# Kernel tuning notes

Hardware: AMD Instinct MI355X
Metric: run time of the kernel (lower is better)

The kernel has to match this reference:

```python
import jax, jax.numpy as jnp
import numpy as np

EPS_NORM = 1e-12  # F.normalize eps
EPS_LOG = 1e-10
COMMITMENT_COST = 0.25


def setup_inputs() -> dict:
    key = jax.random.key(0)
    k1, k2 = jax.random.split(key)
    x = jax.random.normal(k1, (32, 256, 32, 32), dtype=jnp.float32)
    # nn.Embedding weight init: uniform(-1, 1)
    W = jax.random.uniform(k2, (1024, 256), dtype=jnp.float32, minval=-1.0, maxval=1.0)
    return {"x": x, "W": W, "n": 2}


def reference(x, W, n):
    sg = jax.lax.stop_gradient
    # NCHW -> NHWC
    inputs = jnp.transpose(x, (0, 2, 3, 1))
    B, H, Wd, D = inputs.shape
    K = W.shape[0]
    flat = inputs.reshape(-1, D)                       # [N, D]
    N = flat.shape[0]
    # squared euclidean distances via matmul: [N, K]
    distances = (jnp.sum(flat * flat, axis=1, keepdims=True)
                 + jnp.sum(W * W, axis=1)
                 - 2.0 * jnp.matmul(flat, W.T))
    # topk of -distances -> n smallest distances
    neg_vals, encoding_indices = jax.lax.top_k(-distances, n)  # [N, n]
    inv_dist = 1.0 / (-neg_vals)                        # 1/distance, [N, n]
    norm = jnp.maximum(jnp.sqrt(jnp.sum(inv_dist * inv_dist, axis=-1, keepdims=True)), EPS_NORM)
    weights = sg(inv_dist / norm)                       # detached in torch
    # scatter weights into one-hot-ish encodings [N, K]
    rows = jnp.arange(N)[:, None]
    encodings = jnp.zeros((N, K), dtype=flat.dtype).at[rows, encoding_indices].set(weights)
    quantized = jnp.matmul(encodings, W).reshape(B, H, Wd, D)
    e_latent_loss = jnp.mean((sg(quantized) - inputs) ** 2)
    q_latent_loss = jnp.mean((quantized - sg(inputs)) ** 2)
    loss = q_latent_loss + COMMITMENT_COST * e_latent_loss
    # straight-through
    quantized_st = inputs + sg(quantized - inputs)
    avg_probs = jnp.mean(encodings, axis=0)
    perplexity = jnp.exp(-jnp.sum(avg_probs * jnp.log(avg_probs + EPS_LOG)))
    return loss, jnp.transpose(quantized_st, (0, 3, 1, 2)), perplexity, encodings
```

## Files before the change

### kernel.cpp

```cpp
#include <hip/hip_runtime.h>
#include <math.h>

#define NROWS 32768
#define DIMS  256
#define KCODES 1024

typedef __attribute__((ext_vector_type(8))) short short8;
typedef __attribute__((ext_vector_type(4))) float f32x4;

#define SWZW(hw) ((((hw) >> 2) & 7) << 2)

static const size_t OFF_WB     = 8388608;
static const size_t OFF_WNORM  = OFF_WB + 131072;
static const size_t OFF_ENCSUM = OFF_WNORM + 1024;
static const size_t OFF_LOSSP  = OFF_ENCSUM + 1024;
static const size_t OFF_WND    = OFF_LOSSP + 8192;

static const size_t OUT_Q    = 1;
static const size_t OUT_PERP = 8388609;
static const size_t OUT_ENC  = 8388610;

__device__ inline unsigned short f2bf(float f) {
    unsigned int u = __float_as_uint(f);
    unsigned int r = u + 0x7FFFu + ((u >> 16) & 1u);
    return (unsigned short)(r >> 16);
}

__device__ inline float packdi(float d, int code) {
    return __uint_as_float((__float_as_uint(d) & 0xFFFFFC00u) | (unsigned)code);
}

__device__ __forceinline__ void gl_lds16(const void* gsrc, void* ldst) {
    typedef const __attribute__((address_space(1))) unsigned int GU;
    typedef __attribute__((address_space(3))) unsigned int LU;
    __builtin_amdgcn_global_load_lds((GU*)gsrc, (LU*)ldst, 16, 0, 0);
}

__global__ __launch_bounds__(256) void wprep(const float* __restrict__ Wm,
                                             unsigned short* __restrict__ Wb,
                                             float* __restrict__ wnorm,
                                             double* __restrict__ wnormd,
                                             float* __restrict__ enc_sum)
{
    const int r = blockIdx.x * 4 + (threadIdx.x >> 6);
    const int lane = threadIdx.x & 63;
    float4 v = ((const float4*)(Wm + (size_t)r * 256))[lane];
    ushort4 o;
    o.x = f2bf(v.x); o.y = f2bf(v.y); o.z = f2bf(v.z); o.w = f2bf(v.w);
    const int d0 = lane * 4;
    const int kk = d0 >> 5, quad = (d0 >> 3) & 3, jb = d0 & 7;
    const int tt = r >> 4, col = r & 15;
    const size_t idx = (size_t)tt * 4096 + (size_t)((kk * 4 + quad) * 16 + col) * 8 + jb;
    *(ushort4*)(Wb + idx) = o;
    double s = (double)v.x*(double)v.x + (double)v.y*(double)v.y
             + (double)v.z*(double)v.z + (double)v.w*(double)v.w;
    #pragma unroll
    for (int off = 32; off > 0; off >>= 1) s += __shfl_down(s, off);
    if (lane == 0) { wnormd[r] = s; wnorm[r] = (float)s; }
    if (blockIdx.x == 0) {
        #pragma unroll
        for (int q = 0; q < 4; ++q) enc_sum[threadIdx.x * 4 + q] = 0.0f;
    }
}

__global__ __launch_bounds__(256, 4) void gemm_topk_quant(
    const float* __restrict__ x, const unsigned short* __restrict__ Wb,
    const float* __restrict__ wnorm, const double* __restrict__ wnd,
    const float* __restrict__ Wm,
    float* __restrict__ enc_sum,
    float* __restrict__ enc,
    float* __restrict__ outq, float* __restrict__ loss_part)
{
    __shared__ __align__(16) char lds[36864];
    float*  sCd   = (float*)lds;
    int*    mIdx  = (int*)(lds + 13312);
    double* rd    = (double*)(lds + 14336);
    float*  qtile = (float*)lds;
    double* rnr   = (double*)(lds + 33792);
    int*    s0    = (int*)(lds + 34048);
    int*    s1    = (int*)(lds + 34176);
    float*  sw0   = (float*)(lds + 34304);
    float*  sw1   = (float*)(lds + 34432);
    double* sredd = (double*)(lds + 34560);
    float*  xbounce = (float*)(lds + 16384);
    float*  wnLds = (float*)(lds + 32768);

    const int t    = threadIdx.x;
    const int wave = t >> 6;
    const int g    = wave & 1;
    const int h    = wave >> 1;
    const int lane = t & 63;
    const int col  = lane & 15;
    const int quad = lane >> 4;
    const int r0   = blockIdx.x * 32;
    const int b    = r0 >> 10;
    const int hw0  = r0 & 1023;
    const float* xblk = x + (size_t)b * 262144 + hw0;

    const int row = t >> 3;
    const int q8  = t & 7;

    const char* wb_bytes = (const char*)Wb;
    {
        const char* src = wb_bytes + (size_t)(h * 32) * 8192 + g * 4096;
        char* dstl = lds + h * 8192 + g * 4096;
        #pragma unroll
        for (int q = 0; q < 4; ++q)
            gl_lds16(src + q * 1024 + lane * 16, dstl + q * 1024);
        gl_lds16((const char*)wnorm + wave * 1024 + lane * 16,
                 (char*)wnLds + wave * 1024);
    }

    float xs[32];
    short8 af[8];
    const int hwq   = t & 7;
    const int dbase = t >> 3;
    const int arow  = g * 16 + col;
    #pragma unroll
    for (int h2 = 0; h2 < 2; ++h2) {
        float4 xv0, xv1, xv2, xv3;
        {
            const float* xp = xblk + hwq * 4;
            xv0 = *(const float4*)(xp + (size_t)(h2 * 128 +  0 + dbase) * 1024);
            xv1 = *(const float4*)(xp + (size_t)(h2 * 128 + 32 + dbase) * 1024);
            xv2 = *(const float4*)(xp + (size_t)(h2 * 128 + 64 + dbase) * 1024);
            xv3 = *(const float4*)(xp + (size_t)(h2 * 128 + 96 + dbase) * 1024);
        }
        if (h2) __syncthreads();
        #pragma unroll
        for (int rr = 0; rr < 4; ++rr) {
            const float4 xv = (rr == 0) ? xv0 : (rr == 1) ? xv1 : (rr == 2) ? xv2 : xv3;
            const int dloc = rr * 32 + dbase;
            #pragma unroll
            for (int j = 0; j < 4; ++j) {
                const int hw = hwq * 4 + j;
                const float vj = (j == 0) ? xv.x : (j == 1) ? xv.y : (j == 2) ? xv.z : xv.w;
                xbounce[(hw * 128 + dloc) ^ SWZW(hw)] = vj;
            }
        }
        __syncthreads();
        #pragma unroll
        for (int c2 = 0; c2 < 4; ++c2) {
            const int w = (row * 128 + c2 * 32 + q8 * 4) ^ SWZW(row);
            f32x4 v = *(const f32x4*)(xbounce + w);
            xs[(h2 * 4 + c2) * 4 + 0] = v.x;
            xs[(h2 * 4 + c2) * 4 + 1] = v.y;
            xs[(h2 * 4 + c2) * 4 + 2] = v.z;
            xs[(h2 * 4 + c2) * 4 + 3] = v.w;
        }
        #pragma unroll
        for (int kk2 = 0; kk2 < 4; ++kk2) {
            const int dloc = kk2 * 32 + quad * 8;
            const int wA = (arow * 128 + dloc) ^ SWZW(arow);
            const int wB = (arow * 128 + dloc + 4) ^ SWZW(arow);
            f32x4 u = *(const f32x4*)(xbounce + wA);
            f32x4 v = *(const f32x4*)(xbounce + wB);
            short8 f;
            f[0] = (short)f2bf(u.x); f[1] = (short)f2bf(u.y);
            f[2] = (short)f2bf(u.z); f[3] = (short)f2bf(u.w);
            f[4] = (short)f2bf(v.x); f[5] = (short)f2bf(v.y);
            f[6] = (short)f2bf(v.z); f[7] = (short)f2bf(v.w);
            af[h2 * 4 + kk2] = f;
        }
    }
    __syncthreads();

    float m0[4], m1[4], m2[4];
    #pragma unroll
    for (int r = 0; r < 4; ++r) { m0[r] = 3.4e38f; m1[r] = 3.4e38f; m2[r] = 3.4e38f; }

    const f32x4 zero4 = {0.f, 0.f, 0.f, 0.f};
    for (int cc = 0; cc < 32; ++cc) {
        if (cc < 31) {
            const char* src = wb_bytes + (size_t)(h * 32 + cc + 1) * 8192 + g * 4096;
            char* dstl = lds + ((cc + 1) & 1) * 16384 + h * 8192 + g * 4096;
            #pragma unroll
            for (int q = 0; q < 4; ++q)
                gl_lds16(src + q * 1024 + lane * 16, dstl + q * 1024);
        }
        *(f32x4*)(enc + (size_t)(r0 + cc) * KCODES + t * 4) = zero4;

        const char* bb = lds + (cc & 1) * 16384 + h * 8192;
        f32x4 acc_a = {0.f, 0.f, 0.f, 0.f};
        f32x4 acc_b = {0.f, 0.f, 0.f, 0.f};
        #pragma unroll
        for (int kk = 0; kk < 4; ++kk) {
            short8 b0 = *(const short8*)(bb + kk * 1024 + lane * 16);
            short8 b1 = *(const short8*)(bb + (kk + 4) * 1024 + lane * 16);
            acc_a = __builtin_amdgcn_mfma_f32_16x16x32_bf16(af[kk], b0, acc_a, 0, 0, 0);
            acc_b = __builtin_amdgcn_mfma_f32_16x16x32_bf16(af[kk + 4], b1, acc_b, 0, 0, 0);
        }
        const int code0 = h * 512 + cc * 16 + col;
        const float wn0 = wnLds[code0];
        #pragma unroll
        for (int r = 0; r < 4; ++r) {
            float pv0 = packdi(fmaf(-2.0f, acc_a[r] + acc_b[r], wn0), code0);
            m2[r] = __builtin_amdgcn_fmed3f(m1[r], m2[r], pv0);
            m1[r] = __builtin_amdgcn_fmed3f(m0[r], m1[r], pv0);
            m0[r] = fminf(m0[r], pv0);
        }
        __syncthreads();
    }

    #pragma unroll
    for (int r = 0; r < 4; ++r) {
        const int rl = g * 16 + quad * 4 + r;
        const int s  = h * 48 + col * 3;
        sCd[(s + 0) * 34 + rl] = m0[r];
        sCd[(s + 1) * 34 + rl] = m1[r];
        sCd[(s + 2) * 34 + rl] = m2[r];
    }
    __syncthreads();

    {
        float a0 = 3.4e38f, a1 = 3.4e38f, a2 = 3.4e38f, a3 = 3.4e38f,
              a4 = 3.4e38f, a5 = 3.4e38f, a6 = 3.4e38f, a7 = 3.4e38f;
        #pragma unroll
        for (int i = 0; i < 12; ++i) {
            float d = sCd[(q8 * 12 + i) * 34 + row];
            if (d < a7) {
                a7 = d; float tf;
                if (a7 < a6) { tf = a7; a7 = a6; a6 = tf; }
                if (a6 < a5) { tf = a6; a6 = a5; a5 = tf; }
                if (a5 < a4) { tf = a5; a5 = a4; a4 = tf; }
                if (a4 < a3) { tf = a4; a4 = a3; a3 = tf; }
                if (a3 < a2) { tf = a3; a3 = a2; a2 = tf; }
                if (a2 < a1) { tf = a2; a2 = a1; a1 = tf; }
                if (a1 < a0) { tf = a1; a1 = a0; a0 = tf; }
            }
        }
        float sel = 3.4e38f;
        #pragma unroll
        for (int q = 0; q < 8; ++q) {
            float m = a0;
            m = fminf(m, __shfl_xor(m, 1));
            m = fminf(m, __shfl_xor(m, 2));
            m = fminf(m, __shfl_xor(m, 4));
            if (q8 == q) sel = m;
            if (a0 == m) { a0 = a1; a1 = a2; a2 = a3; a3 = a4;
                           a4 = a5; a5 = a6; a6 = a7; a7 = 3.4e38f; }
        }
        mIdx[row * 8 + q8] = (int)(__float_as_uint(sel) & 1023u);
    }
    __syncthreads();

    {
        int cd[8];
        #pragma unroll
        for (int c8 = 0; c8 < 8; ++c8) cd[c8] = mIdx[row * 8 + c8];
        double dot[8];
        #pragma unroll
        for (int c8 = 0; c8 < 8; ++c8) dot[c8] = 0.0;
        double rn = 0.0;
        #pragma unroll
        for (int c = 0; c < 8; ++c) {
            const int d0 = c * 32 + q8 * 4;
            const double x0 = (double)xs[c * 4 + 0];
            const double x1 = (double)xs[c * 4 + 1];
            const double x2 = (double)xs[c * 4 + 2];
            const double x3 = (double)xs[c * 4 + 3];
            rn += x0*x0 + x1*x1 + x2*x2 + x3*x3;
            #pragma unroll
            for (int c8 = 0; c8 < 8; ++c8) {
                const float4 wv = *(const float4*)(Wm + (size_t)cd[c8] * 256 + d0);
                dot[c8] += x0 * (double)wv.x + x1 * (double)wv.y
                         + x2 * (double)wv.z + x3 * (double)wv.w;
            }
        }
        #pragma unroll
        for (int m = 1; m < 8; m <<= 1) {
            #pragma unroll
            for (int c8 = 0; c8 < 8; ++c8) dot[c8] += __shfl_xor(dot[c8], m);
            rn += __shfl_xor(rn, m);
        }
        int myc = 0; double mydot = 0.0;
        #pragma unroll
        for (int c8 = 0; c8 < 8; ++c8)
            if (q8 == c8) { myc = cd[c8]; mydot = dot[c8]; }
        rd[row * 8 + q8] = wnd[myc] - 2.0 * mydot;
        if (q8 == 0) rnr[row] = rn;
    }
    __syncthreads();

    if (t < 32) {
        double rn = rnr[t];
        double d0 = 1e300, d1 = 1e300; int b0 = 1 << 30, b1 = 1 << 30;
        #pragma unroll
        for (int q = 0; q < 8; ++q) {
            double d = rd[t * 8 + q];
            int    c = mIdx[t * 8 + q];
            if (d < d0 || (d == d0 && c < b0)) { d1 = d0; b1 = b0; d0 = d; b0 = c; }
            else if (d < d1 || (d == d1 && c < b1)) { d1 = d; b1 = c; }
        }
        double D0 = rn + d0;
        double D1 = rn + d1;
        double inv0 = 1.0 / D0, inv1 = 1.0 / D1;
        double nrm = sqrt(inv0 * inv0 + inv1 * inv1);
        if (nrm < 1e-12) nrm = 1e-12;
        float w0 = (float)(inv0 / nrm);
        float w1 = (float)(inv1 / nrm);
        s0[t] = b0; s1[t] = b1; sw0[t] = w0; sw1[t] = w1;
        atomicAdd(&enc_sum[b0], w0);
        atomicAdd(&enc_sum[b1], w1);
        enc[(size_t)(r0 + t) * KCODES + b0] = w0;
        enc[(size_t)(r0 + t) * KCODES + b1] = w1;
    }
    __syncthreads();

    double ls = 0.0;
    {
        const int   cA = s0[row], cB = s1[row];
        const float w0 = sw0[row], w1 = sw1[row];
        #pragma unroll
        for (int c = 0; c < 8; ++c) {
            const int dg = c * 32 + q8 * 4;
            const float4 a  = *(const float4*)(Wm + (size_t)cA * 256 + dg);
            const float4 bv = *(const float4*)(Wm + (size_t)cB * 256 + dg);
            float q0 = w0 * a.x + w1 * bv.x;
            float q1 = w0 * a.y + w1 * bv.y;
            float q2 = w0 * a.z + w1 * bv.z;
            float q3 = w0 * a.w + w1 * bv.w;
            float e0 = q0 - xs[c * 4 + 0];
            float e1 = q1 - xs[c * 4 + 1];
            float e2 = q2 - xs[c * 4 + 2];
            float e3 = q3 - xs[c * 4 + 3];
            ls += (double)(e0*e0 + e1*e1 + e2*e2 + e3*e3);
            float* qp = qtile + row * 257 + dg;
            qp[0] = q0; qp[1] = q1; qp[2] = q2; qp[3] = q3;
        }
    }
    __syncthreads();
    #pragma unroll
    for (int p = 0; p < 8; ++p) {
        const int task = p * 256 + t;
        const int cl   = task >> 3;
        const int hq   = task & 7;
        f32x4 v;
        v.x = qtile[(hq * 4 + 0) * 257 + cl];
        v.y = qtile[(hq * 4 + 1) * 257 + cl];
        v.z = qtile[(hq * 4 + 2) * 257 + cl];
        v.w = qtile[(hq * 4 + 3) * 257 + cl];
        *(f32x4*)(outq + ((size_t)(b * 256 + cl)) * 1024 + hw0 + hq * 4) = v;
    }

    #pragma unroll
    for (int off = 32; off > 0; off >>= 1) ls += __shfl_down(ls, off);
    if (lane == 0) sredd[wave] = ls;
    __syncthreads();
    if (t == 0) {
        double s = 0.0;
        #pragma unroll
        for (int w = 0; w < 4; ++w) s += sredd[w];
        loss_part[blockIdx.x] = (float)s;
    }
}

__global__ __launch_bounds__(256) void finalize_k(const float* __restrict__ enc_sum,
                                                  const float* __restrict__ loss_part,
                                                  float* __restrict__ out)
{
    __shared__ double sh[256];
    const int t = threadIdx.x;
    double ls = 0.0;
    for (int i = t; i < 1024; i += 256) ls += (double)loss_part[i];
    sh[t] = ls; __syncthreads();
    for (int s = 128; s > 0; s >>= 1) { if (t < s) sh[t] += sh[t + s]; __syncthreads(); }
    double loss_sum = sh[0];
    __syncthreads();
    double ps = 0.0;
    for (int k = t; k < KCODES; k += 256) {
        double p = (double)enc_sum[k] / (double)NROWS;
        ps += p * log(p + 1e-10);
    }
    sh[t] = ps; __syncthreads();
    for (int s = 128; s > 0; s >>= 1) { if (t < s) sh[t] += sh[t + s]; __syncthreads(); }
    if (t == 0) {
        out[0]        = (float)(1.25 * loss_sum / 8388608.0);
        out[OUT_PERP] = (float)exp(-sh[0]);
    }
}

extern "C" void kernel_launch(void* const* d_in, const int* in_sizes, int n_in,
                              void* d_out, int out_size, void* d_ws, size_t ws_size,
                              hipStream_t stream)
{
    const float* x  = (const float*)d_in[0];
    const float* Wm = (const float*)d_in[1];
    float* out = (float*)d_out;
    float* ws  = (float*)d_ws;

    unsigned short* Wb      = (unsigned short*)(ws + OFF_WB);
    float*          wnorm   = ws + OFF_WNORM;
    float*          enc_sum = ws + OFF_ENCSUM;
    float*          loss_p  = ws + OFF_LOSSP;
    double*         wnd     = (double*)(ws + OFF_WND);

    wprep<<<KCODES / 4, 256, 0, stream>>>(Wm, Wb, wnorm, wnd, enc_sum);
    gemm_topk_quant<<<NROWS / 32, 256, 0, stream>>>(x, Wb, wnorm, wnd, Wm, enc_sum,
                                                    out + OUT_ENC, out + OUT_Q, loss_p);
    finalize_k<<<1, 256, 0, stream>>>(enc_sum, loss_p, out);
}
```

Before: 237.4 us.

## Shrink gemm_topk_quant blocks to 16 rows and 2 waves

Halves the row tile per block from 32 to 16 rows and uses 2 waves instead of 4, doubling the grid to 2048 blocks. Each wave now loads full codebook chunks and computes all 16 rows, and LDS offsets, enc zeroing and the loss partial reduction are reworked to match. The aim is more blocks in flight and better load balance. The cost is twice the per-row codebook streaming and twice the block-level sync overhead.

```diff
diff --git a/kernel.cpp b/kernel.cpp
--- a/kernel.cpp
+++ b/kernel.cpp
@@ -63,7 +63,7 @@
     }
 }
 
-__global__ __launch_bounds__(256, 4) void gemm_topk_quant(
+__global__ __launch_bounds__(128, 2) void gemm_topk_quant(
     const float* __restrict__ x, const unsigned short* __restrict__ Wb,
     const float* __restrict__ wnorm, const double* __restrict__ wnd,
     const float* __restrict__ Wm,
@@ -73,26 +73,24 @@
 {
     __shared__ __align__(16) char lds[36864];
     float*  sCd   = (float*)lds;
-    int*    mIdx  = (int*)(lds + 13312);
-    double* rd    = (double*)(lds + 14336);
+    int*    mIdx  = (int*)(lds + 7424);
+    double* rd    = (double*)(lds + 7936);
+    double* rnr   = (double*)(lds + 8960);
     float*  qtile = (float*)lds;
-    double* rnr   = (double*)(lds + 33792);
-    int*    s0    = (int*)(lds + 34048);
-    int*    s1    = (int*)(lds + 34176);
-    float*  sw0   = (float*)(lds + 34304);
-    float*  sw1   = (float*)(lds + 34432);
-    double* sredd = (double*)(lds + 34560);
+    int*    s0    = (int*)(lds + 16640);
+    int*    s1    = (int*)(lds + 16704);
+    float*  sw0   = (float*)(lds + 16768);
+    float*  sw1   = (float*)(lds + 16832);
+    double* sredd = (double*)(lds + 16896);
     float*  xbounce = (float*)(lds + 16384);
     float*  wnLds = (float*)(lds + 32768);
 
     const int t    = threadIdx.x;
-    const int wave = t >> 6;
-    const int g    = wave & 1;
-    const int h    = wave >> 1;
+    const int h    = t >> 6;
     const int lane = t & 63;
     const int col  = lane & 15;
     const int quad = lane >> 4;
-    const int r0   = blockIdx.x * 32;
+    const int r0   = blockIdx.x * 16;
     const int b    = r0 >> 10;
     const int hw0  = r0 & 1023;
     const float* xblk = x + (size_t)b * 262144 + hw0;
@@ -102,20 +100,21 @@
 
     const char* wb_bytes = (const char*)Wb;
     {
-        const char* src = wb_bytes + (size_t)(h * 32) * 8192 + g * 4096;
-        char* dstl = lds + h * 8192 + g * 4096;
-        #pragma unroll
-        for (int q = 0; q < 4; ++q)
+        const char* src = wb_bytes + (size_t)(h * 32) * 8192;
+        char* dstl = lds + h * 8192;
+        #pragma unroll
+        for (int q = 0; q < 8; ++q)
             gl_lds16(src + q * 1024 + lane * 16, dstl + q * 1024);
-        gl_lds16((const char*)wnorm + wave * 1024 + lane * 16,
-                 (char*)wnLds + wave * 1024);
+        #pragma unroll
+        for (int q = 0; q < 2; ++q)
+            gl_lds16((const char*)wnorm + h * 2048 + q * 1024 + lane * 16,
+                     (char*)wnLds + h * 2048 + q * 1024);
     }
 
     float xs[32];
     short8 af[8];
-    const int hwq   = t & 7;
-    const int dbase = t >> 3;
-    const int arow  = g * 16 + col;
+    const int hwq   = t & 3;
+    const int dbase = t >> 2;
     #pragma unroll
     for (int h2 = 0; h2 < 2; ++h2) {
         float4 xv0, xv1, xv2, xv3;
@@ -151,8 +150,8 @@
         #pragma unroll
         for (int kk2 = 0; kk2 < 4; ++kk2) {
             const int dloc = kk2 * 32 + quad * 8;
-            const int wA = (arow * 128 + dloc) ^ SWZW(arow);
-            const int wB = (arow * 128 + dloc + 4) ^ SWZW(arow);
+            const int wA = (col * 128 + dloc) ^ SWZW(col);
+            const int wB = (col * 128 + dloc + 4) ^ SWZW(col);
             f32x4 u = *(const f32x4*)(xbounce + wA);
             f32x4 v = *(const f32x4*)(xbounce + wB);
             short8 f;
@@ -172,13 +171,13 @@
     const f32x4 zero4 = {0.f, 0.f, 0.f, 0.f};
     for (int cc = 0; cc < 32; ++cc) {
         if (cc < 31) {
-            const char* src = wb_bytes + (size_t)(h * 32 + cc + 1) * 8192 + g * 4096;
-            char* dstl = lds + ((cc + 1) & 1) * 16384 + h * 8192 + g * 4096;
+            const char* src = wb_bytes + (size_t)(h * 32 + cc + 1) * 8192;
+            char* dstl = lds + ((cc + 1) & 1) * 16384 + h * 8192;
             #pragma unroll
-            for (int q = 0; q < 4; ++q)
+            for (int q = 0; q < 8; ++q)
                 gl_lds16(src + q * 1024 + lane * 16, dstl + q * 1024);
         }
-        *(f32x4*)(enc + (size_t)(r0 + cc) * KCODES + t * 4) = zero4;
+        *(f32x4*)(enc + (size_t)(r0 + (cc >> 1)) * KCODES + (cc & 1) * 512 + t * 4) = zero4;
 
         const char* bb = lds + (cc & 1) * 16384 + h * 8192;
         f32x4 acc_a = {0.f, 0.f, 0.f, 0.f};
@@ -204,11 +203,11 @@
 
     #pragma unroll
     for (int r = 0; r < 4; ++r) {
-        const int rl = g * 16 + quad * 4 + r;
+        const int rl = quad * 4 + r;
         const int s  = h * 48 + col * 3;
-        sCd[(s + 0) * 34 + rl] = m0[r];
-        sCd[(s + 1) * 34 + rl] = m1[r];
-        sCd[(s + 2) * 34 + rl] = m2[r];
+        sCd[(s + 0) * 19 + rl] = m0[r];
+        sCd[(s + 1) * 19 + rl] = m1[r];
+        sCd[(s + 2) * 19 + rl] = m2[r];
     }
     __syncthreads();
 
@@ -217,7 +216,7 @@
               a4 = 3.4e38f, a5 = 3.4e38f, a6 = 3.4e38f, a7 = 3.4e38f;
         #pragma unroll
         for (int i = 0; i < 12; ++i) {
-            float d = sCd[(q8 * 12 + i) * 34 + row];
+            float d = sCd[(q8 * 12 + i) * 19 + row];
             if (d < a7) {
                 a7 = d; float tf;
                 if (a7 < a6) { tf = a7; a7 = a6; a6 = tf; }
@@ -282,7 +281,7 @@
     }
     __syncthreads();
 
-    if (t < 32) {
+    if (t < 16) {
         double rn = rnr[t];
         double d0 = 1e300, d1 = 1e300; int b0 = 1 << 30, b1 = 1 << 30;
         #pragma unroll
@@ -332,9 +331,9 @@
     __syncthreads();
     #pragma unroll
     for (int p = 0; p < 8; ++p) {
-        const int task = p * 256 + t;
-        const int cl   = task >> 3;
-        const int hq   = task & 7;
+        const int task = p * 128 + t;
+        const int cl   = task >> 2;
+        const int hq   = task & 3;
         f32x4 v;
         v.x = qtile[(hq * 4 + 0) * 257 + cl];
         v.y = qtile[(hq * 4 + 1) * 257 + cl];
@@ -345,14 +344,9 @@
 
     #pragma unroll
     for (int off = 32; off > 0; off >>= 1) ls += __shfl_down(ls, off);
-    if (lane == 0) sredd[wave] = ls;
-    __syncthreads();
-    if (t == 0) {
-        double s = 0.0;
-        #pragma unroll
-        for (int w = 0; w < 4; ++w) s += sredd[w];
-        loss_part[blockIdx.x] = (float)s;
-    }
+    if (lane == 0) sredd[h] = ls;
+    __syncthreads();
+    if (t == 0) loss_part[blockIdx.x] = (float)(sredd[0] + sredd[1]);
 }
 
 __global__ __launch_bounds__(256) void finalize_k(const float* __restrict__ enc_sum,
@@ -362,7 +356,7 @@
     __shared__ double sh[256];
     const int t = threadIdx.x;
     double ls = 0.0;
-    for (int i = t; i < 1024; i += 256) ls += (double)loss_part[i];
+    for (int i = t; i < 2048; i += 256) ls += (double)loss_part[i];
     sh[t] = ls; __syncthreads();
     for (int s = 128; s > 0; s >>= 1) { if (t < s) sh[t] += sh[t + s]; __syncthreads(); }
     double loss_sum = sh[0];
@@ -396,7 +390,7 @@
     double*         wnd     = (double*)(ws + OFF_WND);
 
     wprep<<<KCODES / 4, 256, 0, stream>>>(Wm, Wb, wnorm, wnd, enc_sum);
-    gemm_topk_quant<<<NROWS / 32, 256, 0, stream>>>(x, Wb, wnorm, wnd, Wm, enc_sum,
+    gemm_topk_quant<<<NROWS / 16, 128, 0, stream>>>(x, Wb, wnorm, wnd, Wm, enc_sum,
                                                     out + OUT_ENC, out + OUT_Q, loss_p);
     finalize_k<<<1, 256, 0, stream>>>(enc_sum, loss_p, out);
 }
```

New measurement: 268.2 us. 1.13x slower.
